# Optimization experiments

Measured on AMD Instinct MI355X. Metric: run time of the kernel, lower is better.

## Reference

```python
import math
import jax, jax.numpy as jnp
import numpy as np

HEADS = 8
D = 128            # model_dim
PE = D // 2        # position_embedding_size (query_positional_score=True)
MAXP = 32          # max_position_embeddings
LN_EPS = 1e-5


def setup_inputs() -> dict:
    key = jax.random.key(0)
    ks = jax.random.split(key, 7)
    bs, h, w = 8, 32, 32
    hidden_state = jax.random.normal(ks[0], (bs, h, w, D), dtype=jnp.float32)
    row_emb = jax.random.normal(ks[1], (2 * MAXP - 1, PE), dtype=jnp.float32) * 0.02
    col_emb = jax.random.normal(ks[2], (2 * MAXP - 1, PE), dtype=jnp.float32) * 0.02
    # torch Linear weights are (out_features, in_features)
    Wq = jax.random.normal(ks[3], (HEADS * D, D), dtype=jnp.float32) / math.sqrt(D)
    Wk = jax.random.normal(ks[4], (HEADS * D, D), dtype=jnp.float32) / math.sqrt(D)
    Wv = jax.random.normal(ks[5], (D, HEADS * D), dtype=jnp.float32) / math.sqrt(HEADS * D)
    bv = jnp.zeros((D,), dtype=jnp.float32)
    ln_g = jnp.ones((D,), dtype=jnp.float32)
    ln_b = jnp.zeros((D,), dtype=jnp.float32)
    return {"hidden_state": hidden_state, "row_emb": row_emb, "col_emb": col_emb,
            "Wq": Wq, "Wk": Wk, "Wv": Wv, "bv": bv, "ln_g": ln_g, "ln_b": ln_b}


def _layer_norm(x, g, b):
    mu = jnp.mean(x, axis=-1, keepdims=True)
    var = jnp.var(x, axis=-1, keepdims=True)
    return (x - mu) * jax.lax.rsqrt(var + LN_EPS) * g + b


def _forward(hidden_state, row_emb, col_emb, Wq, Wk, Wv, bv, ln_g, ln_b):
    bs, h, w, _ = hidden_state.shape
    x = _layer_norm(hidden_state, ln_g, ln_b)  # pre_norm=True
    sqrt_norm = math.sqrt(D)

    # relative indices (static, h == w == 32 here)
    deltas = np.arange(MAXP)[None, :] - np.arange(MAXP)[:, None]
    rel = deltas + MAXP - 1
    row_embeds = row_emb[rel[:w, :w]]  # (w, w, PE)
    col_embeds = col_emb[rel[:h, :h]]  # (h, h, PE)

    # projections; original does .view(bs, w, h, heads, D) on a (bs,h,w,heads*D) tensor
    q = jnp.einsum('bhwc,oc->bhwo', x, Wq).reshape(bs, w, h, HEADS, D)
    k = jnp.einsum('bhwc,oc->bhwo', x, Wk).reshape(bs, w, h, HEADS, D)

    q_row = q[..., :PE]
    q_col = q[..., PE:]
    row_scores = jnp.einsum('bijhd,ikd->bijhk', q_row, row_embeds)
    col_scores = jnp.einsum('bijhd,jld->bijhl', q_col, col_embeds)
    scores = (row_scores[..., :, None] + col_scores[..., None, :]) / sqrt_norm  # bijhkl
    scores = scores.transpose(0, 2, 1, 3, 5, 4)

    content = jnp.einsum('bijhd,bklhd->bijhkl', q, k) / sqrt_norm
    scores = scores + content.transpose(0, 2, 1, 3, 5, 4)  # (bs, h, w, heads, h, w)

    attn_shape = scores.shape
    probs = jax.nn.softmax(scores.reshape(*attn_shape[:-2], -1), axis=-1).reshape(attn_shape)

    # dropout omitted (inference / p=0)
    context = jnp.einsum('bijhkl,bkld->bijhd', probs, x)
    context = context.reshape(bs, h, w, HEADS * D)
    output = jnp.einsum('bhwc,oc->bhwo', context, Wv) + bv + x
    return output, probs


def reference(hidden_state, row_emb, col_emb, Wq, Wk, Wv, bv, ln_g, ln_b):
    return _forward(hidden_state, row_emb, col_emb, Wq, Wk, Wv, bv, ln_g, ln_b)
```

## Files before the change

### kernel.cpp

```cpp
#include <hip/hip_runtime.h>
#include <hip/hip_bf16.h>

#define HEADS 8
#define D 128
#define QSCALE 0.12751743f

typedef unsigned short u16;
typedef unsigned int u32;
typedef __attribute__((ext_vector_type(8))) short short8;
typedef __attribute__((ext_vector_type(4))) float f32x4;

static __device__ inline float sbf2f(short s) {
    return __uint_as_float(((u32)(unsigned short)s) << 16);
}
static __device__ inline u16 f2bf(float f) {
    u32 u = __float_as_uint(f);
    return (u16)((u + 0x7FFFu + ((u >> 16) & 1u)) >> 16);
}
static __device__ inline u32 pk2bf(float a, float b) {
    return (u32)f2bf(a) | ((u32)f2bf(b) << 16);
}
static __device__ inline u32 cvtpk(float a, float b) {
    union { __hip_bfloat162 h; u32 u; } x;
    x.h = __float22bfloat162_rn(make_float2(a, b));
    return x.u;
}
static __device__ inline f32x4 mfma16(short8 a, short8 b, f32x4 c) {
    return __builtin_amdgcn_mfma_f32_16x16x32_bf16(a, b, c, 0, 0, 0);
}
static __device__ inline short8 cvt8(const float* e) {
    f32x4 v0 = *(const f32x4*)e;
    f32x4 v1 = *(const f32x4*)(e + 4);
    union { uint4 u; short8 s; } x;
    x.u = make_uint4(pk2bf(v0[0], v0[1]), pk2bf(v0[2], v0[3]),
                     pk2bf(v1[0], v1[1]), pk2bf(v1[2], v1[3]));
    return x.s;
}
static __device__ __forceinline__ void gload_lds16(const void* g, void* l) {
    __builtin_amdgcn_global_load_lds(
        (const __attribute__((address_space(1))) u32*)g,
        (__attribute__((address_space(3))) u32*)(u32)(uintptr_t)l,
        16, 0, 0);
}

__global__ __launch_bounds__(256) void k_wcvt(const float* __restrict__ Wq,
    const float* __restrict__ Wk, const float* __restrict__ Wv,
    u16* __restrict__ wqk, u16* __restrict__ wv)
{
    int idx = (blockIdx.x * 256 + threadIdx.x) * 4;
    const float* src;
    u16* dst;
    if (idx < 131072)      { src = Wq + idx;           dst = wqk + idx; }
    else if (idx < 262144) { src = Wk + (idx - 131072); dst = wqk + idx; }
    else                   { src = Wv + (idx - 262144); dst = wv + (idx - 262144); }
    f32x4 v = *(const f32x4*)src;
    *(uint2*)dst = make_uint2(pk2bf(v[0], v[1]), pk2bf(v[2], v[3]));
}

__global__ __launch_bounds__(256) void k_lnxt(const float* __restrict__ hs,
    const float* __restrict__ g, const float* __restrict__ bb,
    float* __restrict__ xf, u16* __restrict__ xbf, u16* __restrict__ xt)
{
    __shared__ __align__(16) u16 tl[128][136];
    int b = blockIdx.x, ch = blockIdx.y;
    int tid = threadIdx.x;
    int c4 = (tid & 31) * 4;
    f32x4 g4 = *(const f32x4*)(g + c4);
    f32x4 b4 = *(const f32x4*)(bb + c4);
    const float* src = hs + ((size_t)b * 1024 + ch * 128) * 128;
    #pragma unroll
    for (int it = 0; it < 16; ++it) {
        int p = (tid >> 5) + it * 8;
        f32x4 v = *(const f32x4*)(src + (size_t)p * 128 + c4);
        float s1 = (v[0] + v[1]) + (v[2] + v[3]);
        float s2 = (v[0] * v[0] + v[1] * v[1]) + (v[2] * v[2] + v[3] * v[3]);
        #pragma unroll
        for (int off = 1; off < 32; off <<= 1) {
            s1 += __shfl_xor(s1, off);
            s2 += __shfl_xor(s2, off);
        }
        float mu  = s1 * 0.0078125f;
        float var = s2 * 0.0078125f - mu * mu;
        float inv = rsqrtf(var + 1e-5f);
        f32x4 o;
        #pragma unroll
        for (int q = 0; q < 4; ++q) o[q] = (v[q] - mu) * inv * g4[q] + b4[q];
        size_t row = (size_t)b * 1024 + ch * 128 + p;
        *(f32x4*)(xf + row * 128 + c4) = o;
        *(uint2*)(xbf + row * 128 + c4) = make_uint2(pk2bf(o[0], o[1]), pk2bf(o[2], o[3]));
        tl[c4 + 0][p] = f2bf(o[0]);
        tl[c4 + 1][p] = f2bf(o[1]);
        tl[c4 + 2][p] = f2bf(o[2]);
        tl[c4 + 3][p] = f2bf(o[3]);
    }
    __syncthreads();
    u16* dst = xt + (size_t)b * 131072 + ch * 128;
    #pragma unroll
    for (int i = 0; i < 8; ++i) {
        int d = (tid >> 4) + i * 16, c8 = (tid & 15) * 8;
        *(uint4*)(dst + (size_t)d * 1024 + c8) = *(const uint4*)&tl[d][c8];
    }
}

__global__ __launch_bounds__(256) void k_proj(const u16* __restrict__ xbf,
    const u16* __restrict__ wqk,
    u16* __restrict__ q_bf, u16* __restrict__ kt_bf)
{
    int tid = threadIdx.x;
    int w = tid >> 6, l = tid & 63, h = l >> 4, ln = l & 15;
    int t0 = blockIdx.x * 64 + w * 16;
    int o0 = blockIdx.y * 64;
    short8 a[4];
    #pragma unroll
    for (int s = 0; s < 4; ++s)
        a[s] = *(const short8*)(xbf + (size_t)(t0 + ln) * 128 + s * 32 + h * 8);
    f32x4 acc[4];
    #pragma unroll
    for (int n = 0; n < 4; ++n) acc[n] = f32x4{0.f, 0.f, 0.f, 0.f};
    #pragma unroll
    for (int n = 0; n < 4; ++n) {
        const u16* wsrc = wqk + (size_t)(o0 + n * 16 + ln) * 128;
        #pragma unroll
        for (int s = 0; s < 4; ++s) {
            short8 bf = *(const short8*)(wsrc + s * 32 + h * 8);
            acc[n] = mfma16(a[s], bf, acc[n]);
        }
    }
    bool isq = (o0 < 1024);
    float oscale = isq ? QSCALE : 1.0f;
    int head = (o0 & 1023) >> 7;
    int od_base = (o0 & 127);
    u16* basep = isq ? q_bf : kt_bf;
    #pragma unroll
    for (int n = 0; n < 4; ++n) {
        int d0 = od_base + n * 16 + ln;
        #pragma unroll
        for (int r = 0; r < 4; ++r) {
            int t = t0 + h * 4 + r;
            int b = t >> 10, pos = t & 1023;
            size_t row;
            if (isq) row = (size_t)(b * 8 + head) * 1024 + pos;
            else { int I = pos >> 5, J = pos & 31; row = (size_t)(b * 8 + head) * 1024 + (J * 32 + I); }
            basep[row * 128 + d0] = f2bf(acc[n][r] * oscale);
        }
    }
}

__global__ __launch_bounds__(256) void k_bias(const u16* __restrict__ q_bf,
    const float* __restrict__ row_emb, const float* __restrict__ col_emb,
    float* __restrict__ rbias, float* __restrict__ cbias)
{
    __shared__ __align__(16) float cbf[32][68];
    int tid = threadIdx.x;
    int w = tid >> 6, l = tid & 63, h = l >> 4, ln = l & 15;
    int blk = blockIdx.x;
    int bh = blk >> 5, I = blk & 31;
    const u16* qb = q_bf + ((size_t)bh * 1024 + I * 32) * 128;
    size_t obase = (size_t)blk * 1024;
    if (w < 2) {
        short8 a0 = *(const short8*)(qb + (size_t)(w * 16 + ln) * 128 + h * 8);
        short8 a1 = *(const short8*)(qb + (size_t)(w * 16 + ln) * 128 + 32 + h * 8);
        f32x4 o[2] = {f32x4{0,0,0,0}, f32x4{0,0,0,0}};
        #pragma unroll
        for (int n = 0; n < 2; ++n) {
            int K = n * 16 + ln;
            const float* e = row_emb + (size_t)(K - I + 31) * 64 + h * 8;
            o[n] = mfma16(a0, cvt8(e), o[n]);
            o[n] = mfma16(a1, cvt8(e + 32), o[n]);
        }
        #pragma unroll
        for (int n = 0; n < 2; ++n)
            #pragma unroll
            for (int r = 0; r < 4; ++r)
                rbias[obase + (size_t)(w * 16 + h * 4 + r) * 32 + n * 16 + ln] = o[n][r];
    } else {
        int m = w - 2;
        short8 a0 = *(const short8*)(qb + (size_t)(m * 16 + ln) * 128 + 64 + h * 8);
        short8 a1 = *(const short8*)(qb + (size_t)(m * 16 + ln) * 128 + 96 + h * 8);
        f32x4 o[4] = {f32x4{0,0,0,0}, f32x4{0,0,0,0}, f32x4{0,0,0,0}, f32x4{0,0,0,0}};
        #pragma unroll
        for (int n = 0; n < 4; ++n) {
            int p = n * 16 + ln;
            if (p > 62) p = 62;
            const float* e = col_emb + (size_t)p * 64 + h * 8;
            o[n] = mfma16(a0, cvt8(e), o[n]);
            o[n] = mfma16(a1, cvt8(e + 32), o[n]);
        }
        #pragma unroll
        for (int n = 0; n < 4; ++n)
            #pragma unroll
            for (int r = 0; r < 4; ++r)
                cbf[m * 16 + h * 4 + r][n * 16 + ln] = o[n][r];
    }
    __syncthreads();
    int J = tid >> 3, L0 = (tid & 7) * 4;
    float4 g;
    g.x = cbf[J][L0 + 0 - J + 31];
    g.y = cbf[J][L0 + 1 - J + 31];
    g.z = cbf[J][L0 + 2 - J + 31];
    g.w = cbf[J][L0 + 3 - J + 31];
    *(float4*)(cbias + obase + (size_t)J * 32 + L0) = g;
}

__global__ __launch_bounds__(512, 4) void k_attn(const u16* __restrict__ q_bf,
    const u16* __restrict__ kt_bf, const u16* __restrict__ xt_bf,
    const float* __restrict__ rbias, const float* __restrict__ cbias,
    float* __restrict__ probs, u16* __restrict__ ctx_bf)
{
    __shared__ __align__(16) char KT[8 * 8192];
    __shared__ float wred[256];

    int tid = threadIdx.x;
    int w = tid >> 6, l = tid & 63, h = l >> 4, ln = l & 15;
    int flat = blockIdx.x;
    int bh = flat >> 5, I = flat & 31;
    int b = bh >> 3, head = bh & 7;
    int kk0 = w * 128;
    char* reg = KT + w * 8192;
    const char* ktg = (const char*)(kt_bf + ((size_t)bh * 1024 + kk0) * 128);
    int d0 = w * 16;
    const u16* xb = xt_bf + (size_t)b * 131072 + (size_t)(d0 + ln) * 1024 + h * 8;

    const float* rbase = rbias + (size_t)(bh * 32 + I) * 1024;
    const float* cbase = cbias + (size_t)(bh * 32 + I) * 1024;
    f32x4 rbr[2][2], cbr[2];
    #pragma unroll
    for (int n = 0; n < 2; ++n) {
        int J = n * 16 + ln;
        rbr[n][0] = *(const f32x4*)(rbase + J * 32 + h * 4);
        rbr[n][1] = *(const f32x4*)(rbase + J * 32 + 16 + h * 4);
        cbr[n]    = *(const f32x4*)(cbase + J * 32 + w * 4);
    }
    const u16* qbase = q_bf + ((size_t)bh * 1024 + I * 32) * 128;
    short8 q0[4], q1[4];
    #pragma unroll
    for (int s = 0; s < 4; ++s) {
        q0[s] = *(const short8*)(qbase + (size_t)ln * 128 + s * 32 + h * 8);
        q1[s] = *(const short8*)(qbase + (size_t)(16 + ln) * 128 + s * 32 + h * 8);
    }

    auto stage_chunk = [&](int c, int buf) {
        const char* gs = ktg + c * 4096;
        char* ld = reg + buf * 4096;
        #pragma unroll
        for (int i = 0; i < 4; ++i) {
            int key = ((i * 4 + (l >> 4)) & 7) << 4;
            int o = i * 1024 + l * 16;
            gload_lds16(gs + (o ^ key), ld + i * 1024);
        }
    };
    stage_chunk(0, 0);
    stage_chunk(1, 1);

    f32x4 acc[2][8];
    #pragma unroll
    for (int n = 0; n < 2; ++n)
        #pragma unroll
        for (int t = 0; t < 8; ++t) acc[n][t] = f32x4{0.f, 0.f, 0.f, 0.f};
    int xk = (ln & 7) << 4;
    #pragma unroll
    for (int c = 0; c < 8; ++c) {
        if (c < 7) asm volatile("s_waitcnt vmcnt(4)" ::: "memory");
        else       asm volatile("s_waitcnt vmcnt(0)" ::: "memory");
        const char* cb = reg + (c & 1) * 4096;
        short8 kf[4];
        #pragma unroll
        for (int s = 0; s < 4; ++s)
            kf[s] = *(const short8*)(cb + ((ln * 256 + s * 64 + h * 16) ^ xk));
        asm volatile("s_waitcnt lgkmcnt(0)" ::: "memory");
        __builtin_amdgcn_sched_barrier(0);
        if (c + 2 < 8) stage_chunk(c + 2, c & 1);
        #pragma unroll
        for (int s = 0; s < 4; ++s) {
            acc[0][c] = mfma16(kf[s], q0[s], acc[0][c]);
            acc[1][c] = mfma16(kf[s], q1[s], acc[1][c]);
        }
    }

    #pragma unroll
    for (int n = 0; n < 2; ++n) {
        int J = n * 16 + ln;
        float sum = 0.f;
        #pragma unroll
        for (int t = 0; t < 8; ++t) {
            float cbv = cbr[n][t >> 1];
            float p0 = exp2f(acc[n][t][0] + rbr[n][t & 1][0] + cbv);
            float p1 = exp2f(acc[n][t][1] + rbr[n][t & 1][1] + cbv);
            float p2 = exp2f(acc[n][t][2] + rbr[n][t & 1][2] + cbv);
            float p3 = exp2f(acc[n][t][3] + rbr[n][t & 1][3] + cbv);
            sum += (p0 + p1) + (p2 + p3);
            *(uint2*)(reg + ((J * 256 + t * 32 + h * 8) ^ xk)) =
                make_uint2(cvtpk(p0, p1), cvtpk(p2, p3));
        }
        sum += __shfl_xor(sum, 16);
        sum += __shfl_xor(sum, 32);
        if (l < 16) wred[w * 32 + J] = sum;
    }
    __syncthreads();

    f32x4 sum0 = f32x4{0.f, 0.f, 0.f, 0.f};
    f32x4 sum1 = f32x4{0.f, 0.f, 0.f, 0.f};
    #pragma unroll
    for (int w2 = 0; w2 < 8; ++w2) {
        sum0 += *(const f32x4*)&wred[w2 * 32 + h * 4];
        sum1 += *(const f32x4*)&wred[w2 * 32 + 16 + h * 4];
    }
    int j = tid >> 4;
    float sd = 0.f;
    #pragma unroll
    for (int w2 = 0; w2 < 8; ++w2) sd += wred[w2 * 32 + j];
    float invd = 1.0f / sd;

    f32x4 cacc[2] = {f32x4{0,0,0,0}, f32x4{0,0,0,0}};
    #pragma unroll
    for (int ks = 0; ks < 32; ++ks) {
        short8 xf8 = *(const short8*)(xb + ks * 32);
        #pragma unroll
        for (int m = 0; m < 2; ++m) {
            short8 pa = *(const short8*)(KT + (ks >> 2) * 8192 +
                (((m * 16 + ln) * 256 + (ks & 3) * 64 + h * 16) ^ xk));
            cacc[m] = mfma16(pa, xf8, cacc[m]);
        }
    }
    #pragma unroll
    for (int m = 0; m < 2; ++m)
        #pragma unroll
        for (int r = 0; r < 4; ++r) {
            int J = m * 16 + h * 4 + r;
            float inv = 1.0f / (m ? sum1[r] : sum0[r]);
            ctx_bf[((size_t)(b * 32 + J) * 32 + I) * 1024 + head * 128 + d0 + ln] =
                f2bf(cacc[m][r] * inv);
        }

    {
        float* prow = probs + ((((size_t)(b * 32 + j) * 32 + I) * 8 + head) << 10);
        int jx = (j & 7) << 4;
        #pragma unroll
        for (int i = 0; i < 8; ++i) {
            int kk = i * 128 + (tid & 15) * 8;
            short8 pv = *(const short8*)(KT + i * 8192 +
                            ((j * 256 + (tid & 15) * 16) ^ jx));
            float4 o0, o1;
            o0.x = sbf2f(pv[0]) * invd; o0.y = sbf2f(pv[1]) * invd;
            o0.z = sbf2f(pv[2]) * invd; o0.w = sbf2f(pv[3]) * invd;
            o1.x = sbf2f(pv[4]) * invd; o1.y = sbf2f(pv[5]) * invd;
            o1.z = sbf2f(pv[6]) * invd; o1.w = sbf2f(pv[7]) * invd;
            *(float4*)(prow + kk)     = o0;
            *(float4*)(prow + kk + 4) = o1;
        }
    }
}

__global__ __launch_bounds__(256) void k_out(const u16* __restrict__ ctx_bf,
    const u16* __restrict__ wv_bf, const float* __restrict__ bv,
    const float* __restrict__ xf, float* __restrict__ out)
{
    int tid = threadIdx.x;
    int w = tid >> 6, l = tid & 63, h = l >> 4, ln = l & 15;
    int wm = w >> 1, wn = w & 1;
    int t0 = blockIdx.x * 32 + wm * 16;
    int o0 = blockIdx.y * 64 + wn * 32;
    f32x4 acc[2] = {f32x4{0,0,0,0}, f32x4{0,0,0,0}};
    for (int ks = 0; ks < 32; ++ks) {
        short8 a = *(const short8*)(ctx_bf + (size_t)(t0 + ln) * 1024 + ks * 32 + h * 8);
        #pragma unroll
        for (int nt = 0; nt < 2; ++nt) {
            short8 bb = *(const short8*)(wv_bf + (size_t)(o0 + nt * 16 + ln) * 1024 + ks * 32 + h * 8);
            acc[nt] = mfma16(a, bb, acc[nt]);
        }
    }
    #pragma unroll
    for (int nt = 0; nt < 2; ++nt) {
        int o = o0 + nt * 16 + ln;
        float bvv = bv[o];
        #pragma unroll
        for (int r = 0; r < 4; ++r) {
            int t = t0 + h * 4 + r;
            out[(size_t)t * 128 + o] = acc[nt][r] + bvv + xf[(size_t)t * 128 + o];
        }
    }
}

extern "C" void kernel_launch(void* const* d_in, const int* in_sizes, int n_in,
                              void* d_out, int out_size, void* d_ws, size_t ws_size,
                              hipStream_t stream) {
    (void)in_sizes; (void)n_in; (void)out_size; (void)ws_size;
    const float* hs      = (const float*)d_in[0];
    const float* row_emb = (const float*)d_in[1];
    const float* col_emb = (const float*)d_in[2];
    const float* Wq      = (const float*)d_in[3];
    const float* Wk      = (const float*)d_in[4];
    const float* Wv      = (const float*)d_in[5];
    const float* bv      = (const float*)d_in[6];
    const float* ln_g    = (const float*)d_in[7];
    const float* ln_b    = (const float*)d_in[8];

    float* out   = (float*)d_out;
    float* probs = out + 1048576;

    char* ws = (char*)d_ws;
    float* xf     = (float*)(ws);
    u16*   xbf    = (u16*)(ws + 4194304);
    u16*   q_bf   = (u16*)(ws + 6291456);
    u16*   kt_bf  = (u16*)(ws + 23068672);
    u16*   xt     = (u16*)(ws + 39845888);
    u16*   wqk_bf = (u16*)(ws + 41943040);
    u16*   wv_bf  = (u16*)(ws + 42467328);
    u16*   ctx    = (u16*)(ws + 42729472);
    float* rbias  = (float*)(ws + 59506688);
    float* cbias  = (float*)(ws + 67895296);

    k_wcvt <<<384, 256, 0, stream>>>(Wq, Wk, Wv, wqk_bf, wv_bf);
    k_lnxt <<<dim3(8, 8), 256, 0, stream>>>(hs, ln_g, ln_b, xf, xbf, xt);
    k_proj <<<dim3(128, 32), 256, 0, stream>>>(xbf, wqk_bf, q_bf, kt_bf);
    k_bias <<<2048, 256, 0, stream>>>(q_bf, row_emb, col_emb, rbias, cbias);
    k_attn <<<2048, 512, 0, stream>>>(q_bf, kt_bf, xt, rbias, cbias, probs, ctx);
    k_out  <<<dim3(256, 2), 256, 0, stream>>>(ctx, wv_bf, bv, xf, out);
}
```

Before: 251.5 us.

## Merge weight-convert and layernorm kernels, vectorize projection stores, raise MFMA priority

Combines the weight bf16 conversion and layernorm/transpose kernels into one launch to save a kernel launch and its gap. The projection kernel swaps MFMA operands so each lane holds four consecutive output dims and writes them as one 8-byte store, instead of 16 scattered 2-byte stores with per-element index math. s_setprio is raised around the MFMA loops in the attention kernel so matrix work is favoured over other waves. The merged kernel makes the weight-conversion blocks allocate the layernorm kernel's shared memory, which may limit occupancy for that part.

```diff
diff --git a/kernel.cpp b/kernel.cpp
--- a/kernel.cpp
+++ b/kernel.cpp
@@ -43,27 +43,29 @@
         16, 0, 0);
 }
 
-__global__ __launch_bounds__(256) void k_wcvt(const float* __restrict__ Wq,
-    const float* __restrict__ Wk, const float* __restrict__ Wv,
+__global__ __launch_bounds__(256) void k_init(const float* __restrict__ hs,
+    const float* __restrict__ g, const float* __restrict__ bb,
+    const float* __restrict__ Wq, const float* __restrict__ Wk,
+    const float* __restrict__ Wv,
+    float* __restrict__ xf, u16* __restrict__ xbf, u16* __restrict__ xt,
     u16* __restrict__ wqk, u16* __restrict__ wv)
 {
-    int idx = (blockIdx.x * 256 + threadIdx.x) * 4;
-    const float* src;
-    u16* dst;
-    if (idx < 131072)      { src = Wq + idx;           dst = wqk + idx; }
-    else if (idx < 262144) { src = Wk + (idx - 131072); dst = wqk + idx; }
-    else                   { src = Wv + (idx - 262144); dst = wv + (idx - 262144); }
-    f32x4 v = *(const f32x4*)src;
-    *(uint2*)dst = make_uint2(pk2bf(v[0], v[1]), pk2bf(v[2], v[3]));
-}
-
-__global__ __launch_bounds__(256) void k_lnxt(const float* __restrict__ hs,
-    const float* __restrict__ g, const float* __restrict__ bb,
-    float* __restrict__ xf, u16* __restrict__ xbf, u16* __restrict__ xt)
-{
     __shared__ __align__(16) u16 tl[128][136];
-    int b = blockIdx.x, ch = blockIdx.y;
+    int bid = blockIdx.x;
     int tid = threadIdx.x;
+    if (bid < 384) {
+        int idx = (bid * 256 + tid) * 4;
+        const float* src;
+        u16* dst;
+        if (idx < 131072)      { src = Wq + idx;            dst = wqk + idx; }
+        else if (idx < 262144) { src = Wk + (idx - 131072); dst = wqk + idx; }
+        else                   { src = Wv + (idx - 262144); dst = wv + (idx - 262144); }
+        f32x4 v = *(const f32x4*)src;
+        *(uint2*)dst = make_uint2(pk2bf(v[0], v[1]), pk2bf(v[2], v[3]));
+        return;
+    }
+    int blk = bid - 384;
+    int b = blk >> 3, ch = blk & 7;
     int c4 = (tid & 31) * 4;
     f32x4 g4 = *(const f32x4*)(g + c4);
     f32x4 b4 = *(const f32x4*)(bb + c4);
@@ -110,10 +112,10 @@
     int w = tid >> 6, l = tid & 63, h = l >> 4, ln = l & 15;
     int t0 = blockIdx.x * 64 + w * 16;
     int o0 = blockIdx.y * 64;
-    short8 a[4];
+    short8 tb[4];
     #pragma unroll
     for (int s = 0; s < 4; ++s)
-        a[s] = *(const short8*)(xbf + (size_t)(t0 + ln) * 128 + s * 32 + h * 8);
+        tb[s] = *(const short8*)(xbf + (size_t)(t0 + ln) * 128 + s * 32 + h * 8);
     f32x4 acc[4];
     #pragma unroll
     for (int n = 0; n < 4; ++n) acc[n] = f32x4{0.f, 0.f, 0.f, 0.f};
@@ -122,27 +124,26 @@
         const u16* wsrc = wqk + (size_t)(o0 + n * 16 + ln) * 128;
         #pragma unroll
         for (int s = 0; s < 4; ++s) {
-            short8 bf = *(const short8*)(wsrc + s * 32 + h * 8);
-            acc[n] = mfma16(a[s], bf, acc[n]);
+            short8 wf = *(const short8*)(wsrc + s * 32 + h * 8);
+            acc[n] = mfma16(wf, tb[s], acc[n]);
         }
     }
     bool isq = (o0 < 1024);
-    float oscale = isq ? QSCALE : 1.0f;
+    float os = isq ? QSCALE : 1.0f;
     int head = (o0 & 1023) >> 7;
-    int od_base = (o0 & 127);
+    int od = (o0 & 127);
     u16* basep = isq ? q_bf : kt_bf;
+    int t = t0 + ln;
+    int b = t >> 10, pos = t & 1023;
+    size_t row;
+    if (isq) row = (size_t)(b * 8 + head) * 1024 + pos;
+    else { int I = pos >> 5, J = pos & 31; row = (size_t)(b * 8 + head) * 1024 + (J * 32 + I); }
+    u16* dst = basep + row * 128 + od + h * 4;
     #pragma unroll
     for (int n = 0; n < 4; ++n) {
-        int d0 = od_base + n * 16 + ln;
-        #pragma unroll
-        for (int r = 0; r < 4; ++r) {
-            int t = t0 + h * 4 + r;
-            int b = t >> 10, pos = t & 1023;
-            size_t row;
-            if (isq) row = (size_t)(b * 8 + head) * 1024 + pos;
-            else { int I = pos >> 5, J = pos & 31; row = (size_t)(b * 8 + head) * 1024 + (J * 32 + I); }
-            basep[row * 128 + d0] = f2bf(acc[n][r] * oscale);
-        }
+        *(uint2*)(dst + n * 16) = make_uint2(
+            pk2bf(acc[n][0] * os, acc[n][1] * os),
+            pk2bf(acc[n][2] * os, acc[n][3] * os));
     }
 }
 
@@ -270,11 +271,13 @@
         asm volatile("s_waitcnt lgkmcnt(0)" ::: "memory");
         __builtin_amdgcn_sched_barrier(0);
         if (c + 2 < 8) stage_chunk(c + 2, c & 1);
+        __builtin_amdgcn_s_setprio(1);
         #pragma unroll
         for (int s = 0; s < 4; ++s) {
             acc[0][c] = mfma16(kf[s], q0[s], acc[0][c]);
             acc[1][c] = mfma16(kf[s], q1[s], acc[1][c]);
         }
+        __builtin_amdgcn_s_setprio(0);
     }
 
     #pragma unroll
@@ -312,6 +315,7 @@
     float invd = 1.0f / sd;
 
     f32x4 cacc[2] = {f32x4{0,0,0,0}, f32x4{0,0,0,0}};
+    __builtin_amdgcn_s_setprio(1);
     #pragma unroll
     for (int ks = 0; ks < 32; ++ks) {
         short8 xf8 = *(const short8*)(xb + ks * 32);
@@ -322,6 +326,7 @@
             cacc[m] = mfma16(pa, xf8, cacc[m]);
         }
     }
+    __builtin_amdgcn_s_setprio(0);
     #pragma unroll
     for (int m = 0; m < 2; ++m)
         #pragma unroll
@@ -410,8 +415,8 @@
     float* rbias  = (float*)(ws + 59506688);
     float* cbias  = (float*)(ws + 67895296);
 
-    k_wcvt <<<384, 256, 0, stream>>>(Wq, Wk, Wv, wqk_bf, wv_bf);
-    k_lnxt <<<dim3(8, 8), 256, 0, stream>>>(hs, ln_g, ln_b, xf, xbf, xt);
+    k_init <<<448, 256, 0, stream>>>(hs, ln_g, ln_b, Wq, Wk, Wv,
+                                     xf, xbf, xt, wqk_bf, wv_bf);
     k_proj <<<dim3(128, 32), 256, 0, stream>>>(xbf, wqk_bf, q_bf, kt_bf);
     k_bias <<<2048, 256, 0, stream>>>(q_bf, row_emb, col_emb, rbias, cbias);
     k_attn <<<2048, 512, 0, stream>>>(q_bf, kt_bf, xt, rbias, cbias, probs, ctx);
```

Measured after the change: 250.2 us. Within noise of the previous version (-0.5%).
